# Kernel optimization log

Measured on AMD Instinct MI355X. Metric: run time of the kernel, lower is better.

Reference implementation:

```python
import jax, jax.numpy as jnp
import numpy as np

E = 8
DIMS = [512, 1024, 1024, 512]
BATCH = 2048


def _init_w(key, shape):
    a = np.sqrt(6.0 / (shape[-2] * shape[-1]))
    return jax.random.uniform(key, shape, dtype=jnp.float32, minval=-a, maxval=a)


def setup_inputs() -> dict:
    key = jax.random.key(0)
    ks = jax.random.split(key, 8)
    inp = {
        "weight_blend": jax.random.uniform(ks[0], (BATCH, E), dtype=jnp.float32),
        "x": jax.random.normal(ks[1], (BATCH, DIMS[0]), dtype=jnp.float32),
    }
    for i in range(3):
        inp[f"W{i}"] = _init_w(ks[2 + i], (E, DIMS[i + 1], DIMS[i]))
        inp[f"B{i}"] = jnp.zeros((E, DIMS[i + 1], 1), dtype=jnp.float32)
    return inp


def reference(weight_blend, x, W0, B0, W1, B1, W2, B2):
    Ws = [W0, W1, W2]
    Bs = [B0, B1, B2]
    acts = [jax.nn.elu, jax.nn.elu, None]
    for W, B, act in zip(Ws, Bs, acts):
        # dropout p=0 -> identity
        # blended-expert GEMM: sum_e wb[b,e] * (W[e] @ x[b]) == einsum
        t = jnp.einsum("be,eoi,bi->bo", weight_blend, W, x)
        bias = jnp.einsum("be,eo->bo", weight_blend, B[..., 0])
        x = t + bias
        if act is not None:
            x = act(x)
    return x
```

## Files before the change

### kernel.cpp

```cpp
#include <hip/hip_runtime.h>
#include <math.h>

typedef __attribute__((ext_vector_type(8))) short bf16x8;
typedef __attribute__((ext_vector_type(4))) float f32x4;

#define NEXP 8
#define BATCH 2048

__device__ __forceinline__ unsigned short f2bf(float f) {
    union { float f; unsigned u; } v; v.f = f;
    unsigned r = v.u + 0x7FFFu + ((v.u >> 16) & 1u);
    return (unsigned short)(r >> 16);
}

__device__ __forceinline__ float elu_fast(float v) {
    return v > 0.f ? v : (exp2f(v * 1.4426950408889634f) - 1.0f);
}

__global__ __launch_bounds__(256) void pack_all(
    const float* __restrict__ W0, const float* __restrict__ W1,
    const float* __restrict__ W2, const float* __restrict__ x,
    unsigned short* __restrict__ W0p, unsigned short* __restrict__ W1p,
    unsigned short* __restrict__ W2p, unsigned short* __restrict__ x0p)
{
    __shared__ float T[128 * 36];
    const int bid = blockIdx.x, t = threadIdx.x;

    if (bid < 10240) {
        const float* W; unsigned short* out; int KB, Din, Dout, U, lin;
        if (bid < 2048)      { W = W0; out = W0p; KB = 16; Din = 512;  Dout = 1024; U = 4; lin = bid; }
        else if (bid < 6144) { W = W1; out = W1p; KB = 32; Din = 1024; Dout = 1024; U = 4; lin = bid - 2048; }
        else                 { W = W2; out = W2p; KB = 32; Din = 1024; Dout = 512;  U = 2; lin = bid - 6144; }
        const int e  = lin & 7;
        const int r  = lin >> 3;
        const int kb = r % KB;
        const int nb = r / KB;
        const int N0 = nb * 16 * U;
        const int K0 = kb * 32;
        for (int it = 0; it < U / 2; ++it) {
            const int idx = t + 256 * it;
            const int nl = idx >> 3, k4 = (idx & 7) * 4;
            float4 v = *(const float4*)(W + ((size_t)e * Dout + N0 + nl) * Din + K0 + k4);
            *(float4*)(T + nl * 36 + k4) = v;
        }
        __syncthreads();
        if (t < 64 * U) {
            const int u = t >> 6, l = t & 63;
            const float* p = T + (u * 16 + (l & 15)) * 36 + (l >> 4) * 8;
            bf16x8 h;
            #pragma unroll
            for (int j = 0; j < 8; ++j) h[j] = (short)f2bf(p[j]);
            *(bf16x8*)(out + (size_t)lin * (U * 512) + t * 8) = h;
        }
    } else {
        const int lin = bid - 10240;
        const int kb = lin & 15, mb = lin >> 4;
        for (int it = 0; it < 4; ++it) {
            const int idx = t + 256 * it;
            const int ml = idx >> 3, k4 = (idx & 7) * 4;
            float4 v = *(const float4*)(x + (size_t)(mb * 128 + ml) * 512 + kb * 32 + k4);
            *(float4*)(T + ml * 36 + k4) = v;
        }
        __syncthreads();
        #pragma unroll
        for (int it = 0; it < 2; ++it) {
            const int s = t + 256 * it;
            const int g = s >> 6, l = s & 63;
            const float* p = T + (g * 16 + (l & 15)) * 36 + (l >> 4) * 8;
            bf16x8 h;
            #pragma unroll
            for (int j = 0; j < 8; ++j) h[j] = (short)f2bf(p[j]);
            *(bf16x8*)(x0p + (size_t)lin * 4096 + s * 8) = h;
        }
    }
}

template<int UP>
__device__ __forceinline__ void moe_body128(
    float* lds_f, int bx, int by,
    const unsigned short* __restrict__ Xp,
    const unsigned short* __restrict__ Wp,
    const float* __restrict__ Bias,
    const float* __restrict__ WBl,
    unsigned short* __restrict__ Yout,
    int KB, int Dout, int KBn)
{
    constexpr int PSTR = 68;

    const int tid  = threadIdx.x;
    const int wv   = tid >> 6;
    const int mh   = wv >> 2;
    const int ew   = wv & 3;
    const int l    = tid & 63;
    const int lh   = l >> 4;
    const int ll   = l & 15;
    const int e0   = 2 * ew;
    const int m0   = by * 128 + mh * 64;
    const int n0   = bx * 64;
    const int mb   = by;

    f32x4 acc0[4][4], acc1[4][4];
    #pragma unroll
    for (int t = 0; t < 4; ++t)
        #pragma unroll
        for (int u = 0; u < 4; ++u)
            #pragma unroll
            for (int i = 0; i < 4; ++i) { acc0[t][u][i] = 0.f; acc1[t][u][i] = 0.f; }

    unsigned aoff[4];
    #pragma unroll
    for (int t = 0; t < 4; ++t)
        aoff[t] = (unsigned)(mb * KB) * 8192u + (unsigned)(mh * 4 + t) * 1024u + l * 16u;
    unsigned boff0[4], boff1[4];
    #pragma unroll
    for (int u = 0; u < 4; ++u) {
        const int fn = bx * 4 + u;
        const int nb = fn / UP;
        const int uu = fn % UP;
        boff0[u] = (((unsigned)(nb * KB) * 8 + e0) * UP + uu) * 1024u + l * 16u;
        boff1[u] = boff0[u] + UP * 1024u;
    }
    const unsigned astr = 8192u;
    const unsigned bstr = UP * 8192u;
    const char* xc = (const char*)Xp;
    const char* wc = (const char*)Wp;

    bf16x8 aR[2][4], b0R[2][4], b1R[2][4];

    auto LOAD = [&](int s, int kk) {
        const unsigned ab = (unsigned)kk * astr;
        const unsigned bb = (unsigned)kk * bstr;
        #pragma unroll
        for (int t = 0; t < 4; ++t)
            aR[s][t] = *(const bf16x8*)(xc + aoff[t] + ab);
        #pragma unroll
        for (int u = 0; u < 4; ++u) {
            b0R[s][u] = *(const bf16x8*)(wc + boff0[u] + bb);
            b1R[s][u] = *(const bf16x8*)(wc + boff1[u] + bb);
        }
    };
    auto MF = [&](int s) {
        __builtin_amdgcn_s_setprio(1);
        #pragma unroll
        for (int u = 0; u < 4; ++u)
            #pragma unroll
            for (int t = 0; t < 4; ++t) {
                acc0[t][u] = __builtin_amdgcn_mfma_f32_16x16x32_bf16(aR[s][t], b0R[s][u], acc0[t][u], 0, 0, 0);
                acc1[t][u] = __builtin_amdgcn_mfma_f32_16x16x32_bf16(aR[s][t], b1R[s][u], acc1[t][u], 0, 0, 0);
            }
        __builtin_amdgcn_s_setprio(0);
    };

    LOAD(0, 0);
    for (int kk = 0; kk < KB; kk += 2) {
        if (kk + 1 < KB) LOAD(1, kk + 1);
        MF(0);
        if (kk + 2 < KB) LOAD(0, kk + 2);
        MF(1);
    }

    float bi0[4], bi1[4];
    #pragma unroll
    for (int u = 0; u < 4; ++u) {
        const int n = n0 + u * 16 + ll;
        bi0[u] = Bias[(size_t)e0 * Dout + n];
        bi1[u] = Bias[(size_t)(e0 + 1) * Dout + n];
    }
    float2 wbp[4][4];
    #pragma unroll
    for (int t = 0; t < 4; ++t)
        #pragma unroll
        for (int r = 0; r < 4; ++r) {
            const int lm = 16 * t + 4 * lh + r;
            wbp[t][r] = ((const float2*)(WBl + (size_t)(m0 + lm) * NEXP))[ew];
        }

    float* pb = lds_f + ew * (64 * PSTR);

    #pragma unroll
    for (int h = 0; h < 2; ++h) {
        if (mh == h) {
            #pragma unroll
            for (int t = 0; t < 4; ++t)
                #pragma unroll
                for (int r = 0; r < 4; ++r) {
                    const int lm = 16 * t + 4 * lh + r;
                    #pragma unroll
                    for (int u = 0; u < 4; ++u)
                        pb[lm * PSTR + u * 16 + ll] =
                            wbp[t][r].x * (acc0[t][u][r] + bi0[u]) + wbp[t][r].y * (acc1[t][u][r] + bi1[u]);
                }
        }
        __syncthreads();
        {
            const int kbh = wv >> 2;
            const int g   = wv & 3;
            const int rb  = (g * 16 + ll) * PSTR + kbh * 32 + lh * 8;
            bf16x8 hx;
            #pragma unroll
            for (int j = 0; j < 8; ++j) {
                float v = lds_f[0 * 64 * PSTR + rb + j]
                        + lds_f[1 * 64 * PSTR + rb + j]
                        + lds_f[2 * 64 * PSTR + rb + j]
                        + lds_f[3 * 64 * PSTR + rb + j];
                v = elu_fast(v);
                hx[j] = (short)f2bf(v);
            }
            unsigned short* dst = Yout +
                ((size_t)(mb * KBn + bx * 2 + kbh) * 8 + h * 4 + g) * 512 + l * 8;
            *(bf16x8*)dst = hx;
        }
        if (h == 0) __syncthreads();
    }
}

template<int UP, int NU>
__device__ __forceinline__ void moe_body(
    float* lds_f, int bx, int by,
    const unsigned short* __restrict__ Xp,
    const unsigned short* __restrict__ Wp,
    const float* __restrict__ Bias,
    const float* __restrict__ WBl,
    void* __restrict__ Yout,
    int KB, int Dout, int KBn, int act, int packed_out)
{
    constexpr int PSTR = NU * 16 + 4;

    const int tid  = threadIdx.x;
    const int ew   = tid >> 6;
    const int l    = tid & 63;
    const int lh   = l >> 4;
    const int ll   = l & 15;
    const int e0   = 2 * ew;
    const int m0   = by * 64;
    const int n0   = bx * (NU * 16);
    const int mb   = by >> 1;
    const int half = by & 1;

    f32x4 acc0[4][NU], acc1[4][NU];
    #pragma unroll
    for (int t = 0; t < 4; ++t)
        #pragma unroll
        for (int u = 0; u < NU; ++u)
            #pragma unroll
            for (int i = 0; i < 4; ++i) { acc0[t][u][i] = 0.f; acc1[t][u][i] = 0.f; }

    unsigned aoff[4];
    #pragma unroll
    for (int t = 0; t < 4; ++t)
        aoff[t] = (unsigned)(mb * KB) * 8192u + (unsigned)(half * 4 + t) * 1024u + l * 16u;
    unsigned boff0[NU], boff1[NU];
    #pragma unroll
    for (int u = 0; u < NU; ++u) {
        const int fn = bx * NU + u;
        const int nb = fn / UP;
        const int uu = fn % UP;
        boff0[u] = (((unsigned)(nb * KB) * 8 + e0) * UP + uu) * 1024u + l * 16u;
        boff1[u] = boff0[u] + UP * 1024u;
    }
    const unsigned astr = 8192u;
    const unsigned bstr = UP * 8192u;
    const char* xc = (const char*)Xp;
    const char* wc = (const char*)Wp;

    bf16x8 aR[2][4], b0R[2][NU], b1R[2][NU];

    auto LOAD = [&](int s, int kk) {
        const unsigned ab = (unsigned)kk * astr;
        const unsigned bb = (unsigned)kk * bstr;
        #pragma unroll
        for (int t = 0; t < 4; ++t)
            aR[s][t] = *(const bf16x8*)(xc + aoff[t] + ab);
        #pragma unroll
        for (int u = 0; u < NU; ++u) {
            b0R[s][u] = *(const bf16x8*)(wc + boff0[u] + bb);
            b1R[s][u] = *(const bf16x8*)(wc + boff1[u] + bb);
        }
    };
    auto MF = [&](int s) {
        __builtin_amdgcn_s_setprio(1);
        #pragma unroll
        for (int u = 0; u < NU; ++u)
            #pragma unroll
            for (int t = 0; t < 4; ++t) {
                acc0[t][u] = __builtin_amdgcn_mfma_f32_16x16x32_bf16(aR[s][t], b0R[s][u], acc0[t][u], 0, 0, 0);
                acc1[t][u] = __builtin_amdgcn_mfma_f32_16x16x32_bf16(aR[s][t], b1R[s][u], acc1[t][u], 0, 0, 0);
            }
        __builtin_amdgcn_s_setprio(0);
    };

    LOAD(0, 0);
    for (int kk = 0; kk < KB; kk += 2) {
        if (kk + 1 < KB) LOAD(1, kk + 1);
        MF(0);
        if (kk + 2 < KB) LOAD(0, kk + 2);
        MF(1);
    }

    float bi0[NU], bi1[NU];
    #pragma unroll
    for (int u = 0; u < NU; ++u) {
        const int n = n0 + u * 16 + ll;
        bi0[u] = Bias[(size_t)e0 * Dout + n];
        bi1[u] = Bias[(size_t)(e0 + 1) * Dout + n];
    }
    float2 wbp[4][4];
    #pragma unroll
    for (int t = 0; t < 4; ++t)
        #pragma unroll
        for (int r = 0; r < 4; ++r) {
            const int lm = 16 * t + 4 * lh + r;
            wbp[t][r] = ((const float2*)(WBl + (size_t)(m0 + lm) * NEXP))[ew];
        }

    float* pb = lds_f + ew * (64 * PSTR);
    #pragma unroll
    for (int t = 0; t < 4; ++t)
        #pragma unroll
        for (int r = 0; r < 4; ++r) {
            const int lm = 16 * t + 4 * lh + r;
            #pragma unroll
            for (int u = 0; u < NU; ++u)
                pb[lm * PSTR + u * 16 + ll] =
                    wbp[t][r].x * (acc0[t][u][r] + bi0[u]) + wbp[t][r].y * (acc1[t][u][r] + bi1[u]);
        }
    __syncthreads();

    if (packed_out) {
        if constexpr (NU == 4) {
            #pragma unroll
            for (int it = 0; it < 2; ++it) {
                const int kbh = it;
                const int g   = tid >> 6;
                const int le  = tid & 63;
                const int lhh = le >> 4, lle = le & 15;
                const int rb  = (g * 16 + lle) * PSTR + kbh * 32 + lhh * 8;
                bf16x8 h;
                #pragma unroll
                for (int j = 0; j < 8; ++j) {
                    float v = lds_f[0 * 64 * PSTR + rb + j]
                            + lds_f[1 * 64 * PSTR + rb + j]
                            + lds_f[2 * 64 * PSTR + rb + j]
                            + lds_f[3 * 64 * PSTR + rb + j];
                    if (act) v = elu_fast(v);
                    h[j] = (short)f2bf(v);
                }
                unsigned short* dst = (unsigned short*)Yout +
                    ((size_t)(mb * KBn + bx * 2 + kbh) * 8 + half * 4 + g) * 512 + le * 8;
                *(bf16x8*)dst = h;
            }
        }
    } else {
        constexpr int F4R = NU * 4;
        #pragma unroll
        for (int it = 0; it < NU; ++it) {
            const int idx = tid + 256 * it;
            const int row = idx / F4R;
            const int c4  = (idx % F4R) * 4;
            const int rb  = row * PSTR + c4;
            float4 s  = *(const float4*)(lds_f + 0 * 64 * PSTR + rb);
            float4 q1 = *(const float4*)(lds_f + 1 * 64 * PSTR + rb);
            float4 q2 = *(const float4*)(lds_f + 2 * 64 * PSTR + rb);
            float4 q3 = *(const float4*)(lds_f + 3 * 64 * PSTR + rb);
            s.x += q1.x + q2.x + q3.x;
            s.y += q1.y + q2.y + q3.y;
            s.z += q1.z + q2.z + q3.z;
            s.w += q1.w + q2.w + q3.w;
            if (act) {
                s.x = elu_fast(s.x);
                s.y = elu_fast(s.y);
                s.z = elu_fast(s.z);
                s.w = elu_fast(s.w);
            }
            *(float4*)((float*)Yout + (size_t)(m0 + row) * Dout + n0 + c4) = s;
        }
    }
}

__device__ __forceinline__ void swz256(int& bx, int& by) {
    const int bid = blockIdx.x;
    const int xcd = bid & 7;
    const int loc = bid >> 3;
    bx = xcd * 2 + (loc & 1);
    by = loc >> 1;
}
__device__ __forceinline__ void swz_pair(int& bx, int& by) {
    const int bid = blockIdx.x;
    const int xcd = bid & 7;
    const int loc = bid >> 3;
    bx = xcd * 2 + (loc & 1);
    by = loc >> 1;
}

__global__ __launch_bounds__(512, 2) void moe_l0(
    const unsigned short* __restrict__ Xp, const unsigned short* __restrict__ Wp,
    const float* __restrict__ Bias, const float* __restrict__ WBl,
    unsigned short* __restrict__ Yout, int KB, int Dout, int KBn)
{
    __shared__ __align__(16) float lds_f[4 * 64 * 68];
    int bx, by; swz256(bx, by);
    moe_body128<4>(lds_f, bx, by, Xp, Wp, Bias, WBl, Yout, KB, Dout, KBn);
}
__global__ __launch_bounds__(512, 2) void moe_l1(
    const unsigned short* __restrict__ Xp, const unsigned short* __restrict__ Wp,
    const float* __restrict__ Bias, const float* __restrict__ WBl,
    unsigned short* __restrict__ Yout, int KB, int Dout, int KBn)
{
    __shared__ __align__(16) float lds_f[4 * 64 * 68];
    int bx, by; swz256(bx, by);
    moe_body128<4>(lds_f, bx, by, Xp, Wp, Bias, WBl, Yout, KB, Dout, KBn);
}
__global__ __launch_bounds__(256, 2) void moe_l2(
    const unsigned short* __restrict__ Xp, const unsigned short* __restrict__ Wp,
    const float* __restrict__ Bias, const float* __restrict__ WBl,
    void* __restrict__ Yout, int KB, int Dout, int KBn, int act, int packed_out)
{
    __shared__ __align__(16) float lds_f[4 * 64 * 36];
    int bx, by; swz_pair(bx, by);
    moe_body<2, 2>(lds_f, bx, by, Xp, Wp, Bias, WBl, Yout, KB, Dout, KBn, act, packed_out);
}

#define BM 64
#define BNF 64
#define BKF 16
#define PAD 4

__global__ __launch_bounds__(256) void moe_layer_f32(
    const float* __restrict__ X, const float* __restrict__ W,
    const float* __restrict__ Bias, const float* __restrict__ WB,
    float* __restrict__ Y, int Din, int Dout, int act)
{
    __shared__ float As[BKF][BM + PAD];
    __shared__ float Bs[BKF][BNF + PAD];
    const int tid = threadIdx.x;
    const int tm = tid >> 4, tn = tid & 15;
    const int m0 = blockIdx.y * BM, n0 = blockIdx.x * BNF;
    const int lr = tid >> 2, lc = (tid & 3) << 2;
    float acc[4][4] = {};
    const float* xrow  = X  + (size_t)(m0 + lr) * Din;
    const float* wbrow = WB + (size_t)(m0 + lr) * NEXP;
    const float* wrow0 = W  + (size_t)(n0 + lr) * Din;
    for (int e = 0; e < NEXP; ++e) {
        const float wbe = wbrow[e];
        const float* wrow = wrow0 + (size_t)e * Dout * Din;
        for (int k0 = 0; k0 < Din; k0 += BKF) {
            float4 av = *(const float4*)(xrow + k0 + lc);
            float4 bv = *(const float4*)(wrow + k0 + lc);
            __syncthreads();
            As[lc+0][lr] = av.x*wbe; As[lc+1][lr] = av.y*wbe;
            As[lc+2][lr] = av.z*wbe; As[lc+3][lr] = av.w*wbe;
            Bs[lc+0][lr] = bv.x; Bs[lc+1][lr] = bv.y;
            Bs[lc+2][lr] = bv.z; Bs[lc+3][lr] = bv.w;
            __syncthreads();
            #pragma unroll
            for (int k = 0; k < BKF; ++k) {
                float4 a = *(const float4*)&As[k][tm << 2];
                float4 b = *(const float4*)&Bs[k][tn << 2];
                acc[0][0]+=a.x*b.x; acc[0][1]+=a.x*b.y; acc[0][2]+=a.x*b.z; acc[0][3]+=a.x*b.w;
                acc[1][0]+=a.y*b.x; acc[1][1]+=a.y*b.y; acc[1][2]+=a.y*b.z; acc[1][3]+=a.y*b.w;
                acc[2][0]+=a.z*b.x; acc[2][1]+=a.z*b.y; acc[2][2]+=a.z*b.z; acc[2][3]+=a.z*b.w;
                acc[3][0]+=a.w*b.x; acc[3][1]+=a.w*b.y; acc[3][2]+=a.w*b.z; acc[3][3]+=a.w*b.w;
            }
        }
    }
    #pragma unroll
    for (int im = 0; im < 4; ++im) {
        const int m = m0 + (tm << 2) + im;
        const float* wbm = WB + (size_t)m * NEXP;
        float wv[NEXP];
        #pragma unroll
        for (int e = 0; e < NEXP; ++e) wv[e] = wbm[e];
        #pragma unroll
        for (int in = 0; in < 4; ++in) {
            const int n = n0 + (tn << 2) + in;
            float bsum = 0.f;
            #pragma unroll
            for (int e = 0; e < NEXP; ++e) bsum += wv[e] * Bias[(size_t)e * Dout + n];
            float v = acc[im][in] + bsum;
            if (act) v = v > 0.f ? v : expm1f(v);
            acc[im][in] = v;
        }
        float4 o = make_float4(acc[im][0], acc[im][1], acc[im][2], acc[im][3]);
        *(float4*)(Y + (size_t)m * Dout + n0 + (tn << 2)) = o;
    }
}

extern "C" void kernel_launch(void* const* d_in, const int* in_sizes, int n_in,
                              void* d_out, int out_size, void* d_ws, size_t ws_size,
                              hipStream_t stream)
{
    (void)in_sizes; (void)n_in; (void)out_size;
    const float* wb = (const float*)d_in[0];
    const float* x  = (const float*)d_in[1];
    const float* W0 = (const float*)d_in[2];
    const float* B0 = (const float*)d_in[3];
    const float* W1 = (const float*)d_in[4];
    const float* B1 = (const float*)d_in[5];
    const float* W2 = (const float*)d_in[6];
    const float* B2 = (const float*)d_in[7];
    float* out = (float*)d_out;

    const size_t NW0 = (size_t)8*1024*512, NW1 = (size_t)8*1024*1024, NW2 = (size_t)8*512*1024;
    const size_t NX0 = (size_t)BATCH*512, NX1 = (size_t)BATCH*1024;
    const size_t need = (NW0 + NW1 + NW2 + NX0 + 2 * NX1) * 2;

    if (ws_size >= need) {
        unsigned short* W0p = (unsigned short*)d_ws;
        unsigned short* W1p = W0p + NW0;
        unsigned short* W2p = W1p + NW1;
        unsigned short* x0p = W2p + NW2;
        unsigned short* x1p = x0p + NX0;
        unsigned short* x2p = x1p + NX1;
        pack_all<<<10496, 256, 0, stream>>>(W0, W1, W2, x, W0p, W1p, W2p, x0p);
        moe_l0<<<256, 512, 0, stream>>>(x0p, W0p, B0, wb, x1p, 16, 1024, 32);
        moe_l1<<<256, 512, 0, stream>>>(x1p, W1p, B1, wb, x2p, 32, 1024, 32);
        moe_l2<<<512, 256, 0, stream>>>(x2p, W2p, B2, wb, out, 32, 512,  0, 0, 0);
    } else {
        float* x1 = (float*)d_ws;
        float* x2 = x1 + (size_t)BATCH * 1024;
        moe_layer_f32<<<dim3(1024/BNF, BATCH/BM), 256, 0, stream>>>(x,  W0, B0, wb, x1, 512,  1024, 1);
        moe_layer_f32<<<dim3(1024/BNF, BATCH/BM), 256, 0, stream>>>(x1, W1, B1, wb, x2, 1024, 1024, 1);
        moe_layer_f32<<<dim3(512/BNF,  BATCH/BM), 256, 0, stream>>>(x2, W2, B2, wb, out, 1024, 512,  0);
    }
}
```

Measured before the change: 192.3 us.

## Stage MoE layer-0/1 tiles through LDS via async global_load_lds double buffering

Layers 0 and 1 previously loaded A and B fragments from global memory straight into registers, with each wave loading its own copy of the shared A tiles. Now each wave issues five direct global-to-LDS 16-byte loads per k-step into a double-buffered 80 KB LDS region, and all waves then read their fragments from LDS. This removes redundant global loads of the shared A tiles and lowers register pressure from the register double buffer. In exchange it adds a block-wide barrier every k-step and uses much more LDS, which may limit the launch-bounds target of two blocks per CU.

```diff
diff --git a/kernel.cpp b/kernel.cpp
--- a/kernel.cpp
+++ b/kernel.cpp
@@ -15,6 +15,12 @@
 
 __device__ __forceinline__ float elu_fast(float v) {
     return v > 0.f ? v : (exp2f(v * 1.4426950408889634f) - 1.0f);
+}
+
+__device__ __forceinline__ void gl_lds(const char* g, char* l) {
+    __builtin_amdgcn_global_load_lds(
+        (const __attribute__((address_space(1))) void*)g,
+        (__attribute__((address_space(3))) void*)l, 16, 0, 0);
 }
 
 __global__ __launch_bounds__(256) void pack_all(
@@ -76,8 +82,8 @@
 }
 
 template<int UP>
-__device__ __forceinline__ void moe_body128(
-    float* lds_f, int bx, int by,
+__device__ __forceinline__ void moe_stage(
+    char* smem, int bx, int by,
     const unsigned short* __restrict__ Xp,
     const unsigned short* __restrict__ Wp,
     const float* __restrict__ Bias,
@@ -86,6 +92,7 @@
     int KB, int Dout, int KBn)
 {
     constexpr int PSTR = 68;
+    constexpr unsigned BUFB = 40 * 1024;
 
     const int tid  = threadIdx.x;
     const int wv   = tid >> 6;
@@ -107,58 +114,66 @@
             #pragma unroll
             for (int i = 0; i < 4; ++i) { acc0[t][u][i] = 0.f; acc1[t][u][i] = 0.f; }
 
-    unsigned aoff[4];
-    #pragma unroll
-    for (int t = 0; t < 4; ++t)
-        aoff[t] = (unsigned)(mb * KB) * 8192u + (unsigned)(mh * 4 + t) * 1024u + l * 16u;
-    unsigned boff0[4], boff1[4];
-    #pragma unroll
-    for (int u = 0; u < 4; ++u) {
-        const int fn = bx * 4 + u;
-        const int nb = fn / UP;
-        const int uu = fn % UP;
-        boff0[u] = (((unsigned)(nb * KB) * 8 + e0) * UP + uu) * 1024u + l * 16u;
-        boff1[u] = boff0[u] + UP * 1024u;
-    }
-    const unsigned astr = 8192u;
-    const unsigned bstr = UP * 8192u;
     const char* xc = (const char*)Xp;
     const char* wc = (const char*)Wp;
-
-    bf16x8 aR[2][4], b0R[2][4], b1R[2][4];
-
-    auto LOAD = [&](int s, int kk) {
-        const unsigned ab = (unsigned)kk * astr;
-        const unsigned bb = (unsigned)kk * bstr;
+    const int fidbase = wv * 5;
+    const char* gp[5]; unsigned kst[5];
+    #pragma unroll
+    for (int s = 0; s < 5; ++s) {
+        const int fid = fidbase + s;
+        if (fid < 8) {
+            gp[s]  = xc + (unsigned)(mb * KB) * 8192u + (unsigned)fid * 1024u + l * 16u;
+            kst[s] = 8192u;
+        } else {
+            const int idx = fid - 8;
+            const int e   = 2 * (idx >> 3) + ((idx >> 2) & 1);
+            const int u   = idx & 3;
+            const int fn  = bx * 4 + u;
+            const int nb  = fn / UP;
+            const int uu  = fn % UP;
+            gp[s]  = wc + (unsigned)((nb * KB * 8 + e) * UP + uu) * 1024u + l * 16u;
+            kst[s] = UP * 8192u;
+        }
+    }
+
+    auto STAGE = [&](int b, int kk) {
+        char* lb = smem + (unsigned)b * BUFB + (unsigned)fidbase * 1024u;
+        #pragma unroll
+        for (int s = 0; s < 5; ++s)
+            gl_lds(gp[s] + (unsigned)kk * kst[s], lb + s * 1024);
+    };
+
+    auto COMPUTE = [&](int b) {
+        const char* sb = smem + (unsigned)b * BUFB;
+        bf16x8 aR[4], b0R[4], b1R[4];
         #pragma unroll
         for (int t = 0; t < 4; ++t)
-            aR[s][t] = *(const bf16x8*)(xc + aoff[t] + ab);
+            aR[t] = *(const bf16x8*)(sb + (mh * 4 + t) * 1024 + l * 16);
         #pragma unroll
         for (int u = 0; u < 4; ++u) {
-            b0R[s][u] = *(const bf16x8*)(wc + boff0[u] + bb);
-            b1R[s][u] = *(const bf16x8*)(wc + boff1[u] + bb);
-        }
-    };
-    auto MF = [&](int s) {
+            b0R[u] = *(const bf16x8*)(sb + (8 + ew * 8 + u) * 1024 + l * 16);
+            b1R[u] = *(const bf16x8*)(sb + (8 + ew * 8 + 4 + u) * 1024 + l * 16);
+        }
         __builtin_amdgcn_s_setprio(1);
         #pragma unroll
         for (int u = 0; u < 4; ++u)
             #pragma unroll
             for (int t = 0; t < 4; ++t) {
-                acc0[t][u] = __builtin_amdgcn_mfma_f32_16x16x32_bf16(aR[s][t], b0R[s][u], acc0[t][u], 0, 0, 0);
-                acc1[t][u] = __builtin_amdgcn_mfma_f32_16x16x32_bf16(aR[s][t], b1R[s][u], acc1[t][u], 0, 0, 0);
+                acc0[t][u] = __builtin_amdgcn_mfma_f32_16x16x32_bf16(aR[t], b0R[u], acc0[t][u], 0, 0, 0);
+                acc1[t][u] = __builtin_amdgcn_mfma_f32_16x16x32_bf16(aR[t], b1R[u], acc1[t][u], 0, 0, 0);
             }
         __builtin_amdgcn_s_setprio(0);
     };
 
-    LOAD(0, 0);
-    for (int kk = 0; kk < KB; kk += 2) {
-        if (kk + 1 < KB) LOAD(1, kk + 1);
-        MF(0);
-        if (kk + 2 < KB) LOAD(0, kk + 2);
-        MF(1);
-    }
-
+    STAGE(0, 0);
+    __syncthreads();
+    for (int kk = 0; kk < KB; ++kk) {
+        if (kk + 1 < KB) STAGE((kk + 1) & 1, kk + 1);
+        COMPUTE(kk & 1);
+        __syncthreads();
+    }
+
+    float* epi = (float*)smem;
     float bi0[4], bi1[4];
     #pragma unroll
     for (int u = 0; u < 4; ++u) {
@@ -175,8 +190,7 @@
             wbp[t][r] = ((const float2*)(WBl + (size_t)(m0 + lm) * NEXP))[ew];
         }
 
-    float* pb = lds_f + ew * (64 * PSTR);
-
+    float* pb = epi + ew * (64 * PSTR);
     #pragma unroll
     for (int h = 0; h < 2; ++h) {
         if (mh == h) {
@@ -199,10 +213,10 @@
             bf16x8 hx;
             #pragma unroll
             for (int j = 0; j < 8; ++j) {
-                float v = lds_f[0 * 64 * PSTR + rb + j]
-                        + lds_f[1 * 64 * PSTR + rb + j]
-                        + lds_f[2 * 64 * PSTR + rb + j]
-                        + lds_f[3 * 64 * PSTR + rb + j];
+                float v = epi[0 * 64 * PSTR + rb + j]
+                        + epi[1 * 64 * PSTR + rb + j]
+                        + epi[2 * 64 * PSTR + rb + j]
+                        + epi[3 * 64 * PSTR + rb + j];
                 v = elu_fast(v);
                 hx[j] = (short)f2bf(v);
             }
@@ -397,18 +411,18 @@
     const float* __restrict__ Bias, const float* __restrict__ WBl,
     unsigned short* __restrict__ Yout, int KB, int Dout, int KBn)
 {
-    __shared__ __align__(16) float lds_f[4 * 64 * 68];
+    __shared__ __align__(16) char smem[2 * 40 * 1024];
     int bx, by; swz256(bx, by);
-    moe_body128<4>(lds_f, bx, by, Xp, Wp, Bias, WBl, Yout, KB, Dout, KBn);
+    moe_stage<4>(smem, bx, by, Xp, Wp, Bias, WBl, Yout, KB, Dout, KBn);
 }
 __global__ __launch_bounds__(512, 2) void moe_l1(
     const unsigned short* __restrict__ Xp, const unsigned short* __restrict__ Wp,
     const float* __restrict__ Bias, const float* __restrict__ WBl,
     unsigned short* __restrict__ Yout, int KB, int Dout, int KBn)
 {
-    __shared__ __align__(16) float lds_f[4 * 64 * 68];
+    __shared__ __align__(16) char smem[2 * 40 * 1024];
     int bx, by; swz256(bx, by);
-    moe_body128<4>(lds_f, bx, by, Xp, Wp, Bias, WBl, Yout, KB, Dout, KBn);
+    moe_stage<4>(smem, bx, by, Xp, Wp, Bias, WBl, Yout, KB, Dout, KBn);
 }
 __global__ __launch_bounds__(256, 2) void moe_l2(
     const unsigned short* __restrict__ Xp, const unsigned short* __restrict__ Wp,
```

After: 186.9 us. 2.8% less time.
